# Performance work log

Hardware: AMD Instinct MI355X
Metric: run time of the kernel (lower is better)

The kernel has to match this reference:

```python
import jax, jax.numpy as jnp
import numpy as np
import math

CHANNELS = 128
NUM_NODES = 170
LENGTH = 12
BATCH = 128


def setup_inputs() -> dict:
    key = jax.random.key(0)
    k_x, k_es = jax.random.split(key)
    x = jax.random.normal(k_x, (BATCH, CHANNELS, NUM_NODES, LENGTH), dtype=jnp.float32)
    # xavier_uniform for E_s [channels, num_nodes]
    bound = math.sqrt(6.0 / (CHANNELS + NUM_NODES))
    E_s = jax.random.uniform(k_es, (CHANNELS, NUM_NODES), dtype=jnp.float32,
                             minval=-bound, maxval=bound)
    return {"x": x, "E_s": E_s}


def reference(x, E_s):
    # x: [B, C, N, T], E_s: [C, M] with M == N (num_nodes)
    # Note: the original also computes E_t = x * E_tod**2, which is dead code
    # (never used in the returned value), so it is omitted here.
    C = x.shape[1]
    # node embeddings: sum over channel and time -> [B, N, M]
    E_d = jnp.tanh(jnp.einsum('bcnt,cm->bnm', x, E_s))
    # node-node similarity: contract over the M (embedding) axis -> [B, N, N]
    scores = jax.nn.relu(jnp.einsum('bnm,bkm->bnk', E_d, E_d) / jnp.sqrt(jnp.float32(C)))
    A_adp = jax.nn.softmax(scores, axis=-1)  # [B, N, N]
    A_mean = A_adp.mean(axis=0)              # [N, N]
    return (A_mean > 0.5).astype(jnp.float32)
```

## Files before the change

### kernel.cpp

```cpp
#include <hip/hip_runtime.h>
#include <math.h>

#define NB 128
#define NC 128
#define NN 170
#define NT 12
#define MP 176
#define XSTR 176
#define MEST 192

#define EST_SZ ((size_t)MEST * NC)
#define XS_SZ  ((size_t)NB * NC * XSTR)
#define P_SZ   ((size_t)NB * NN * MP)

typedef _Float16 h8 __attribute__((ext_vector_type(8)));
typedef __fp16   g2 __attribute__((ext_vector_type(2)));
typedef float    f4 __attribute__((ext_vector_type(4)));

__device__ __forceinline__ float fast_tanh(float x) {
    float cx = fminf(fmaxf(x, -15.f), 15.f);
    float e  = __expf(2.f * cx);
    return (e - 1.f) * __builtin_amdgcn_rcpf(e + 1.f);
}

__global__ __launch_bounds__(256) void k1_tsum_est(const float* __restrict__ x,
                                                   const float* __restrict__ Es,
                                                   _Float16* __restrict__ xs,
                                                   _Float16* __restrict__ Est) {
    const int bid = blockIdx.x;
    if (bid < 5440) {
        unsigned tid = bid * 256u + threadIdx.x;
        unsigned bc = tid / 85u;
        unsigned p  = tid - bc * 85u;
        const float4* q = reinterpret_cast<const float4*>(
            x + (size_t)bc * (NN * NT) + (size_t)p * (2 * NT));
        float4 f0 = q[0], f1 = q[1], f2 = q[2];
        float4 f3 = q[3], f4v = q[4], f5 = q[5];
        float s0 = ((f0.x + f0.y) + (f0.z + f0.w))
                 + ((f1.x + f1.y) + (f1.z + f1.w))
                 + ((f2.x + f2.y) + (f2.z + f2.w));
        float s1 = ((f3.x + f3.y) + (f3.z + f3.w))
                 + ((f4v.x + f4v.y) + (f4v.z + f4v.w))
                 + ((f5.x + f5.y) + (f5.z + f5.w));
        g2 pk = __builtin_amdgcn_cvt_pkrtz(s0, s1);
        *reinterpret_cast<g2*>(xs + (size_t)bc * XSTR + 2 * p) = pk;
        if (p < 3)
            *reinterpret_cast<unsigned*>(xs + (size_t)bc * XSTR + 170 + 2 * p) = 0u;
    } else {
        int idx = (bid - 5440) * 256 + threadIdx.x;
        int m = idx >> 7, c = idx & 127;
        Est[idx] = (m < NN) ? (_Float16)Es[c * NN + m] : (_Float16)0.f;
    }
}

#define ATSW(row, c)  ((row) * 128 + (((((c) >> 3) ^ ((row) & 7)) << 3) | ((c) & 7)))
#define EDSW(row, m)  ((row) * 192 + (((((m) >> 3) ^ ((row) & 7)) << 3) | ((m) & 7)))
#define SCSTR 204

__global__ __launch_bounds__(256) void k23_fused(const _Float16* __restrict__ xs,
                                                 const _Float16* __restrict__ Est,
                                                 _Float16* __restrict__ P) {
    const int h = blockIdx.x, b = blockIdx.y;
    const int t = threadIdx.x;
    const int lane = t & 63, wave = t >> 6;
    const int l15 = lane & 15, quad = lane >> 4;
    const int r0 = h * 96;

    __shared__ __align__(16) _Float16 EdL[192 * 192];
    __shared__ __align__(16) char UN[192 * 128 * 2];
    _Float16* At = (_Float16*)UN;
    float*    Sc = (float*)UN;

    const _Float16* __restrict__ xsb = xs + (size_t)b * NC * XSTR;
    #pragma unroll
    for (int it = 0; it < 12; ++it) {
        int g  = t + it * 256;
        int gg = g >> 7;
        int c  = g & 127;
        int n0g = gg * 8;
        h8 v = {};
        if (n0g < XSTR)
            v = *reinterpret_cast<const h8*>(xsb + (size_t)c * XSTR + n0g);
        #pragma unroll
        for (int j = 0; j < 8; ++j)
            At[ATSW(n0g + j, c)] = v[j];
    }
    __syncthreads();

    {
        h8 a[3][4];
        #pragma unroll
        for (int rt = 0; rt < 3; ++rt)
            #pragma unroll
            for (int kk = 0; kk < 4; ++kk) {
                int row = wave * 48 + rt * 16 + l15;
                int cg  = kk * 4 + quad;
                a[rt][kk] = *reinterpret_cast<const h8*>(
                    &At[row * 128 + ((cg ^ (row & 7)) << 3)]);
            }
        #pragma unroll 2
        for (int ct = 0; ct < 12; ++ct) {
            h8 bfr[4];
            #pragma unroll
            for (int kk = 0; kk < 4; ++kk)
                bfr[kk] = *reinterpret_cast<const h8*>(
                    Est + (size_t)(ct * 16 + l15) * NC + kk * 32 + quad * 8);
            f4 acc1[3] = {};
            #pragma unroll
            for (int kk = 0; kk < 4; ++kk)
                #pragma unroll
                for (int rt = 0; rt < 3; ++rt)
                    acc1[rt] = __builtin_amdgcn_mfma_f32_16x16x32_f16(
                        a[rt][kk], bfr[kk], acc1[rt], 0, 0, 0);
            #pragma unroll
            for (int rt = 0; rt < 3; ++rt)
                #pragma unroll
                for (int reg = 0; reg < 4; ++reg) {
                    int n = wave * 48 + rt * 16 + quad * 4 + reg;
                    int m = ct * 16 + l15;
                    EdL[EDSW(n, m)] = (_Float16)fast_tanh(acc1[rt][reg]);
                }
        }
    }
    __syncthreads();

    f4 acc2[6][3] = {};
    #pragma unroll
    for (int mc = 0; mc < 192; mc += 32) {
        h8 a2[6], b2[3];
        #pragma unroll
        for (int rt = 0; rt < 6; ++rt) {
            int row = r0 + rt * 16 + l15;
            int mg  = (mc >> 3) + quad;
            a2[rt] = *reinterpret_cast<const h8*>(
                &EdL[row * 192 + ((mg ^ (row & 7)) << 3)]);
        }
        #pragma unroll
        for (int ci = 0; ci < 3; ++ci) {
            int row = (wave * 3 + ci) * 16 + l15;
            int mg  = (mc >> 3) + quad;
            b2[ci] = *reinterpret_cast<const h8*>(
                &EdL[row * 192 + ((mg ^ (row & 7)) << 3)]);
        }
        #pragma unroll
        for (int rt = 0; rt < 6; ++rt)
            #pragma unroll
            for (int ci = 0; ci < 3; ++ci)
                acc2[rt][ci] = __builtin_amdgcn_mfma_f32_16x16x32_f16(
                    a2[rt], b2[ci], acc2[rt][ci], 0, 0, 0);
    }

    const float scale = 0.08838834764831845f;
    #pragma unroll
    for (int p = 0; p < 2; ++p) {
        __syncthreads();
        #pragma unroll
        for (int rt3 = 0; rt3 < 3; ++rt3) {
            int rt = p * 3 + rt3;
            #pragma unroll
            for (int ci = 0; ci < 3; ++ci) {
                int col = (wave * 3 + ci) * 16 + l15;
                #pragma unroll
                for (int reg = 0; reg < 4; ++reg) {
                    int rloc = rt3 * 16 + quad * 4 + reg;
                    Sc[rloc * SCSTR + col] = fmaxf(acc2[rt][ci][reg] * scale, 0.f);
                }
            }
        }
        __syncthreads();
        for (int rr = 0; rr < 12; ++rr) {
            int r = wave * 12 + rr;
            int n = r0 + p * 48 + r;
            if (n >= NN) continue;
            float v0 = Sc[r * SCSTR + lane];
            float v1 = Sc[r * SCSTR + lane + 64];
            int  k2i = lane + 128;
            bool has2 = (k2i < NN);
            float v2 = has2 ? Sc[r * SCSTR + k2i] : -1.f;
            float m = fmaxf(fmaxf(v0, v1), v2);
            #pragma unroll
            for (int off = 32; off; off >>= 1) m = fmaxf(m, __shfl_xor(m, off, 64));
            float e0 = __expf(v0 - m);
            float e1 = __expf(v1 - m);
            float e2 = has2 ? __expf(v2 - m) : 0.f;
            float s = e0 + e1 + e2;
            #pragma unroll
            for (int off = 32; off; off >>= 1) s += __shfl_xor(s, off, 64);
            float inv = 1.f / s;
            _Float16* Pr = P + ((size_t)(b * NN + n)) * MP;
            Pr[lane]      = (_Float16)(e0 * inv);
            Pr[lane + 64] = (_Float16)(e1 * inv);
            if (has2) Pr[k2i] = (_Float16)(e2 * inv);
        }
    }
}

__global__ __launch_bounds__(256) void k4_mean_thresh(const _Float16* __restrict__ P,
                                                      float* __restrict__ out) {
    int p = blockIdx.x * 256 + threadIdx.x;
    if (p >= NN * NN) return;
    int n = p / NN, k = p - n * NN;
    const _Float16* base = P + (size_t)n * MP + k;
    float s0 = 0.f, s1 = 0.f, s2 = 0.f, s3 = 0.f;
    #pragma unroll
    for (int b = 0; b < NB; b += 4) {
        s0 += (float)base[(size_t)(b + 0) * NN * MP];
        s1 += (float)base[(size_t)(b + 1) * NN * MP];
        s2 += (float)base[(size_t)(b + 2) * NN * MP];
        s3 += (float)base[(size_t)(b + 3) * NN * MP];
    }
    float s = (s0 + s1) + (s2 + s3);
    out[p] = (s * (1.f / 128.f) > 0.5f) ? 1.f : 0.f;
}

extern "C" void kernel_launch(void* const* d_in, const int* in_sizes, int n_in,
                              void* d_out, int out_size, void* d_ws, size_t ws_size,
                              hipStream_t stream) {
    const float* x  = (const float*)d_in[0];
    const float* Es = (const float*)d_in[1];
    float* out = (float*)d_out;

    _Float16* Est = (_Float16*)d_ws;
    _Float16* xs  = Est + EST_SZ;
    _Float16* P   = xs + XS_SZ;

    k1_tsum_est<<<5536, 256, 0, stream>>>(x, Es, xs, Est);
    k23_fused<<<dim3(2, 128), 256, 0, stream>>>(xs, Est, P);
    k4_mean_thresh<<<113, 256, 0, stream>>>(P, out);
}
```

Measured before the change: 227.3 us.

## Fuse time-sum reduction into main kernel with one 1024-thread block per batch

Removes the separate time-summation kernel and its fp16 intermediate buffer; the fused kernel now streams x directly, reduces over time through an LDS staging buffer, and builds the transposed A tile in shared memory. The grid changes from two 256-thread blocks per batch to a single 1024-thread block per batch, removing the duplicated first GEMM and tanh work that each half-block previously did. The trade-off is only 128 blocks on the device, each with large LDS use and frequent block-wide barriers during the x load, which may leave bandwidth underused while reading the dominant input.

```diff
diff --git a/kernel.cpp b/kernel.cpp
--- a/kernel.cpp
+++ b/kernel.cpp
@@ -5,16 +5,13 @@
 #define NC 128
 #define NN 170
 #define NT 12
+#define NP 192
 #define MP 176
-#define XSTR 176
-#define MEST 192
-
-#define EST_SZ ((size_t)MEST * NC)
-#define XS_SZ  ((size_t)NB * NC * XSTR)
+
+#define EST_SZ ((size_t)NP * NC)
 #define P_SZ   ((size_t)NB * NN * MP)
 
 typedef _Float16 h8 __attribute__((ext_vector_type(8)));
-typedef __fp16   g2 __attribute__((ext_vector_type(2)));
 typedef float    f4 __attribute__((ext_vector_type(4)));
 
 __device__ __forceinline__ float fast_tanh(float x) {
@@ -23,127 +20,118 @@
     return (e - 1.f) * __builtin_amdgcn_rcpf(e + 1.f);
 }
 
-__global__ __launch_bounds__(256) void k1_tsum_est(const float* __restrict__ x,
-                                                   const float* __restrict__ Es,
-                                                   _Float16* __restrict__ xs,
-                                                   _Float16* __restrict__ Est) {
-    const int bid = blockIdx.x;
-    if (bid < 5440) {
-        unsigned tid = bid * 256u + threadIdx.x;
-        unsigned bc = tid / 85u;
-        unsigned p  = tid - bc * 85u;
-        const float4* q = reinterpret_cast<const float4*>(
-            x + (size_t)bc * (NN * NT) + (size_t)p * (2 * NT));
-        float4 f0 = q[0], f1 = q[1], f2 = q[2];
-        float4 f3 = q[3], f4v = q[4], f5 = q[5];
-        float s0 = ((f0.x + f0.y) + (f0.z + f0.w))
-                 + ((f1.x + f1.y) + (f1.z + f1.w))
-                 + ((f2.x + f2.y) + (f2.z + f2.w));
-        float s1 = ((f3.x + f3.y) + (f3.z + f3.w))
-                 + ((f4v.x + f4v.y) + (f4v.z + f4v.w))
-                 + ((f5.x + f5.y) + (f5.z + f5.w));
-        g2 pk = __builtin_amdgcn_cvt_pkrtz(s0, s1);
-        *reinterpret_cast<g2*>(xs + (size_t)bc * XSTR + 2 * p) = pk;
-        if (p < 3)
-            *reinterpret_cast<unsigned*>(xs + (size_t)bc * XSTR + 170 + 2 * p) = 0u;
-    } else {
-        int idx = (bid - 5440) * 256 + threadIdx.x;
-        int m = idx >> 7, c = idx & 127;
-        Est[idx] = (m < NN) ? (_Float16)Es[c * NN + m] : (_Float16)0.f;
-    }
+__global__ __launch_bounds__(256) void kprep_est(const float* __restrict__ Es,
+                                                 _Float16* __restrict__ Est) {
+    int idx = blockIdx.x * 256 + threadIdx.x;
+    int m = idx >> 7, c = idx & 127;
+    Est[idx] = (m < NN) ? (_Float16)Es[c * NN + m] : (_Float16)0.f;
 }
 
 #define ATSW(row, c)  ((row) * 128 + (((((c) >> 3) ^ ((row) & 7)) << 3) | ((c) & 7)))
 #define EDSW(row, m)  ((row) * 192 + (((((m) >> 3) ^ ((row) & 7)) << 3) | ((m) & 7)))
 #define SCSTR 204
 
-__global__ __launch_bounds__(256) void k23_fused(const _Float16* __restrict__ xs,
+__global__ __launch_bounds__(1024) void kA_fused(const float* __restrict__ x,
                                                  const _Float16* __restrict__ Est,
                                                  _Float16* __restrict__ P) {
-    const int h = blockIdx.x, b = blockIdx.y;
+    const int b = blockIdx.x;
     const int t = threadIdx.x;
     const int lane = t & 63, wave = t >> 6;
     const int l15 = lane & 15, quad = lane >> 4;
-    const int r0 = h * 96;
-
+    const int wr = wave >> 2, wc = wave & 3;
+
+    __shared__ __align__(16) float    L[16 * 510];
+    __shared__ __align__(16) char     UN[192 * 128 * 2];
     __shared__ __align__(16) _Float16 EdL[192 * 192];
-    __shared__ __align__(16) char UN[192 * 128 * 2];
     _Float16* At = (_Float16*)UN;
     float*    Sc = (float*)UN;
 
-    const _Float16* __restrict__ xsb = xs + (size_t)b * NC * XSTR;
-    #pragma unroll
-    for (int it = 0; it < 12; ++it) {
-        int g  = t + it * 256;
-        int gg = g >> 7;
-        int c  = g & 127;
-        int n0g = gg * 8;
-        h8 v = {};
-        if (n0g < XSTR)
-            v = *reinterpret_cast<const h8*>(xsb + (size_t)c * XSTR + n0g);
-        #pragma unroll
-        for (int j = 0; j < 8; ++j)
-            At[ATSW(n0g + j, c)] = v[j];
-    }
-    __syncthreads();
+    const float4* xb = reinterpret_cast<const float4*>(x + (size_t)b * NC * NN * NT);
+    for (int r8 = 0; r8 < 8; ++r8) {
+        float4 vv[8];
+        #pragma unroll
+        for (int it = 0; it < 8; ++it) {
+            int s = t + it * 1024;
+            vv[it] = (s < 8160) ? xb[(size_t)r8 * 8160 + s]
+                                : make_float4(0.f, 0.f, 0.f, 0.f);
+        }
+        #pragma unroll
+        for (int it = 0; it < 8; ++it) {
+            int s = t + it * 1024;
+            if (s < 8160)
+                L[s] = (vv[it].x + vv[it].y) + (vv[it].z + vv[it].w);
+        }
+        __syncthreads();
+        #pragma unroll
+        for (int it = 0; it < 3; ++it) {
+            int idx = t + it * 1024;
+            int n = idx >> 4, cc = idx & 15;
+            float s = 0.f;
+            if (n < NN)
+                s = L[cc * 510 + 3 * n] + L[cc * 510 + 3 * n + 1]
+                  + L[cc * 510 + 3 * n + 2];
+            At[ATSW(n, r8 * 16 + cc)] = (_Float16)s;
+        }
+        __syncthreads();
+    }
 
     {
-        h8 a[3][4];
-        #pragma unroll
-        for (int rt = 0; rt < 3; ++rt)
-            #pragma unroll
-            for (int kk = 0; kk < 4; ++kk) {
-                int row = wave * 48 + rt * 16 + l15;
-                int cg  = kk * 4 + quad;
-                a[rt][kk] = *reinterpret_cast<const h8*>(
-                    &At[row * 128 + ((cg ^ (row & 7)) << 3)]);
+        f4 acc1[3][3] = {};
+        #pragma unroll
+        for (int kk = 0; kk < 4; ++kk) {
+            int ks = kk * 32 + quad * 8;
+            h8 a[3], bf[3];
+            #pragma unroll
+            for (int rt = 0; rt < 3; ++rt) {
+                int row = wr * 48 + rt * 16 + l15;
+                a[rt] = *reinterpret_cast<const h8*>(
+                    &At[row * 128 + (((ks >> 3) ^ (row & 7)) << 3)]);
             }
-        #pragma unroll 2
-        for (int ct = 0; ct < 12; ++ct) {
-            h8 bfr[4];
-            #pragma unroll
-            for (int kk = 0; kk < 4; ++kk)
-                bfr[kk] = *reinterpret_cast<const h8*>(
-                    Est + (size_t)(ct * 16 + l15) * NC + kk * 32 + quad * 8);
-            f4 acc1[3] = {};
-            #pragma unroll
-            for (int kk = 0; kk < 4; ++kk)
-                #pragma unroll
-                for (int rt = 0; rt < 3; ++rt)
-                    acc1[rt] = __builtin_amdgcn_mfma_f32_16x16x32_f16(
-                        a[rt][kk], bfr[kk], acc1[rt], 0, 0, 0);
+            #pragma unroll
+            for (int ci = 0; ci < 3; ++ci) {
+                int m = wc * 48 + ci * 16 + l15;
+                bf[ci] = *reinterpret_cast<const h8*>(Est + (size_t)m * NC + ks);
+            }
             #pragma unroll
             for (int rt = 0; rt < 3; ++rt)
                 #pragma unroll
+                for (int ci = 0; ci < 3; ++ci)
+                    acc1[rt][ci] = __builtin_amdgcn_mfma_f32_16x16x32_f16(
+                        a[rt], bf[ci], acc1[rt][ci], 0, 0, 0);
+        }
+        #pragma unroll
+        for (int rt = 0; rt < 3; ++rt)
+            #pragma unroll
+            for (int ci = 0; ci < 3; ++ci) {
+                int m = wc * 48 + ci * 16 + l15;
+                #pragma unroll
                 for (int reg = 0; reg < 4; ++reg) {
-                    int n = wave * 48 + rt * 16 + quad * 4 + reg;
-                    int m = ct * 16 + l15;
-                    EdL[EDSW(n, m)] = (_Float16)fast_tanh(acc1[rt][reg]);
+                    int n = wr * 48 + rt * 16 + quad * 4 + reg;
+                    EdL[EDSW(n, m)] = (_Float16)fast_tanh(acc1[rt][ci][reg]);
                 }
-        }
+            }
     }
     __syncthreads();
 
-    f4 acc2[6][3] = {};
-    #pragma unroll
+    f4 acc2[3][3] = {};
+    #pragma unroll 2
     for (int mc = 0; mc < 192; mc += 32) {
-        h8 a2[6], b2[3];
-        #pragma unroll
-        for (int rt = 0; rt < 6; ++rt) {
-            int row = r0 + rt * 16 + l15;
-            int mg  = (mc >> 3) + quad;
+        int mg = (mc >> 3) + quad;
+        h8 a2[3], b2[3];
+        #pragma unroll
+        for (int rt = 0; rt < 3; ++rt) {
+            int row = wr * 48 + rt * 16 + l15;
             a2[rt] = *reinterpret_cast<const h8*>(
                 &EdL[row * 192 + ((mg ^ (row & 7)) << 3)]);
         }
         #pragma unroll
         for (int ci = 0; ci < 3; ++ci) {
-            int row = (wave * 3 + ci) * 16 + l15;
-            int mg  = (mc >> 3) + quad;
+            int row = wc * 48 + ci * 16 + l15;
             b2[ci] = *reinterpret_cast<const h8*>(
                 &EdL[row * 192 + ((mg ^ (row & 7)) << 3)]);
         }
         #pragma unroll
-        for (int rt = 0; rt < 6; ++rt)
+        for (int rt = 0; rt < 3; ++rt)
             #pragma unroll
             for (int ci = 0; ci < 3; ++ci)
                 acc2[rt][ci] = __builtin_amdgcn_mfma_f32_16x16x32_f16(
@@ -151,26 +139,26 @@
     }
 
     const float scale = 0.08838834764831845f;
-    #pragma unroll
-    for (int p = 0; p < 2; ++p) {
-        __syncthreads();
-        #pragma unroll
-        for (int rt3 = 0; rt3 < 3; ++rt3) {
-            int rt = p * 3 + rt3;
-            #pragma unroll
-            for (int ci = 0; ci < 3; ++ci) {
-                int col = (wave * 3 + ci) * 16 + l15;
+    for (int p = 0; p < 4; ++p) {
+        __syncthreads();
+        if (wr == p) {
+            #pragma unroll
+            for (int rt = 0; rt < 3; ++rt)
                 #pragma unroll
-                for (int reg = 0; reg < 4; ++reg) {
-                    int rloc = rt3 * 16 + quad * 4 + reg;
-                    Sc[rloc * SCSTR + col] = fmaxf(acc2[rt][ci][reg] * scale, 0.f);
+                for (int ci = 0; ci < 3; ++ci) {
+                    int col = wc * 48 + ci * 16 + l15;
+                    #pragma unroll
+                    for (int reg = 0; reg < 4; ++reg) {
+                        int rloc = rt * 16 + quad * 4 + reg;
+                        Sc[rloc * SCSTR + col] = fmaxf(acc2[rt][ci][reg] * scale, 0.f);
+                    }
                 }
-            }
-        }
-        __syncthreads();
-        for (int rr = 0; rr < 12; ++rr) {
-            int r = wave * 12 + rr;
-            int n = r0 + p * 48 + r;
+        }
+        __syncthreads();
+        #pragma unroll
+        for (int rr = 0; rr < 3; ++rr) {
+            int r = wave * 3 + rr;
+            int n = p * 48 + r;
             if (n >= NN) continue;
             float v0 = Sc[r * SCSTR + lane];
             float v1 = Sc[r * SCSTR + lane + 64];
@@ -221,10 +209,9 @@
     float* out = (float*)d_out;
 
     _Float16* Est = (_Float16*)d_ws;
-    _Float16* xs  = Est + EST_SZ;
-    _Float16* P   = xs + XS_SZ;
-
-    k1_tsum_est<<<5536, 256, 0, stream>>>(x, Es, xs, Est);
-    k23_fused<<<dim3(2, 128), 256, 0, stream>>>(xs, Est, P);
+    _Float16* P   = Est + EST_SZ;
+
+    kprep_est<<<96, 256, 0, stream>>>(Es, Est);
+    kA_fused<<<128, 1024, 0, stream>>>(x, Est, P);
     k4_mean_thresh<<<113, 256, 0, stream>>>(P, out);
 }
```

New measurement: 220.5 us. 3.0% less time.
